# Kernel optimization log

Measured on AMD Instinct MI355X. Metric: run time of the kernel, lower is better.

## Reference

```python
import jax, jax.numpy as jnp
import numpy as np

B, T, C, H, D, W = 4, 4096, 1024, 16, 64, 128  # batch, seq, n_embd, n_head, head_dim, window
NB = T // W  # number of query blocks
EPS = 1e-6


def _rms(x, w):
    # RMSNorm over last dim
    return x * jax.lax.rsqrt(jnp.mean(x * x, axis=-1, keepdims=True) + EPS) * w


def _rope(x, pos_ids):
    # MRoPE: pos_ids [T,3]; axis_id maps each freq to one of 3 axes
    inv_freq = 1.0 / (1e6 ** (jnp.arange(0, D, 2, dtype=jnp.float32) / D))  # [D/2]
    axis_id = jnp.arange(D // 2) % 3
    positions = pos_ids[:, axis_id].astype(jnp.float32)  # [T, D/2]
    freqs = positions * inv_freq  # [T, D/2]
    emb = jnp.concatenate([freqs, freqs], axis=-1)  # [T, D]
    cos = jnp.cos(emb)[None, None]  # [1,1,T,D]
    sin = jnp.sin(emb)[None, None]
    x1, x2 = x[..., : D // 2], x[..., D // 2 :]
    rot = jnp.concatenate([-x2, x1], axis=-1)
    return x * cos + rot * sin


def setup_inputs() -> dict:
    key = jax.random.key(0)
    ks = jax.random.split(key, 3)
    x = jax.random.normal(ks[0], (B, T, C), jnp.float32)
    pos = jnp.arange(T, dtype=jnp.int32)
    pos_ids = jnp.stack([pos, pos, pos], axis=-1)  # [T,3] text positions
    w_attn = jax.random.normal(ks[1], (C, C + 2 * D), jnp.float32) * 0.02
    w_proj = jax.random.normal(ks[2], (C, C), jnp.float32) * 0.02
    q_norm_w = jnp.ones((D,), jnp.float32)
    k_norm_w = jnp.ones((D,), jnp.float32)
    return {"x": x, "pos_ids": pos_ids, "w_attn": w_attn, "w_proj": w_proj,
            "q_norm_w": q_norm_w, "k_norm_w": k_norm_w}


def reference(x, pos_ids, w_attn, w_proj, q_norm_w, k_norm_w):
    # fused qkv projection (torch Linear without bias; weight stored [in,out])
    qkv = x @ w_attn  # [B,T,C+2D]
    q = qkv[..., :C].reshape(B, T, H, D).transpose(0, 2, 1, 3)  # [B,H,T,D]
    k = qkv[..., C : C + D][:, None]  # [B,1,T,D] single KV head (MQA)
    v = qkv[..., C + D :][:, None]  # [B,1,T,D]
    q = _rope(_rms(q, q_norm_w), pos_ids)
    k = _rope(_rms(k, k_norm_w), pos_ids)
    # sliding-window attention (q >= kv and q - kv <= W), computed in blocks of W
    qb = q.reshape(B, H, NB, W, D)
    kb = k.reshape(B, NB, W, D)
    vb = v.reshape(B, NB, W, D)
    kp = jnp.concatenate([jnp.zeros_like(kb[:, :1]), kb[:, :-1]], axis=1)  # prev k block
    vp = jnp.concatenate([jnp.zeros_like(vb[:, :1]), vb[:, :-1]], axis=1)
    kv_k = jnp.concatenate([kp, kb], axis=2)  # [B,NB,2W,D]
    kv_v = jnp.concatenate([vp, vb], axis=2)
    n = jnp.arange(NB)[:, None, None]
    qr = jnp.arange(W)[None, :, None]
    kr = jnp.arange(2 * W)[None, None, :]
    q_abs = n * W + qr
    kv_abs = (n - 1) * W + kr
    mask = (q_abs >= kv_abs) & (q_abs - kv_abs <= W) & (kv_abs >= 0)  # [NB,W,2W]
    scores = jnp.einsum("bhnqd,bnkd->bhnqk", qb, kv_k) / jnp.sqrt(jnp.float32(D))
    scores = jnp.where(mask[None, None], scores, -1e30)
    attn = jax.nn.softmax(scores, axis=-1)
    y = jnp.einsum("bhnqk,bnkd->bhnqd", attn, kv_v)  # [B,H,NB,W,D]
    y = y.reshape(B, H, T, D).transpose(0, 2, 1, 3).reshape(B, T, C)
    return y @ w_proj
```

## Files before the change

kernel.cpp:

```cpp
#include <hip/hip_runtime.h>


typedef __attribute__((ext_vector_type(8))) short short8;
typedef __attribute__((ext_vector_type(4))) float f32x4;
typedef __attribute__((ext_vector_type(16))) float f32x16;
typedef __attribute__((ext_vector_type(4))) unsigned uint4v;

#define DEV static __device__ __forceinline__

DEV unsigned short f2bf(float f) {
  unsigned u = __builtin_bit_cast(unsigned, f);
  u += 0x7fffu + ((u >> 16) & 1u);
  return (unsigned short)(u >> 16);
}
DEV float bf2f(unsigned short s) {
  unsigned u = ((unsigned)s) << 16;
  return __builtin_bit_cast(float, u);
}
DEV unsigned cvtpk(float a, float b) {
  unsigned r;
  asm("v_cvt_pk_bf16_f32 %0, %1, %2" : "=v"(r) : "v"(a), "v"(b));
  return r;
}

DEV f32x4 mfma16(short8 a, short8 b, f32x4 c) {
  return __builtin_amdgcn_mfma_f32_16x16x32_bf16(a, b, c, 0, 0, 0);
}
DEV f32x16 mfma32(short8 a, short8 b, f32x16 c) {
  return __builtin_amdgcn_mfma_f32_32x32x16_bf16(a, b, c, 0, 0, 0);
}

DEV void gload16(const void* g, void* l) {
  __builtin_amdgcn_global_load_lds(
      (const __attribute__((address_space(1))) unsigned int*)(unsigned long long)g,
      (__attribute__((address_space(3))) unsigned int*)(unsigned int)(unsigned long long)l,
      16, 0, 0);
}

__global__ __launch_bounds__(256) void k_prep(const float* __restrict__ x,
                                              short* __restrict__ xb,
                                              const float* __restrict__ wa,
                                              short* __restrict__ wabt,
                                              const float* __restrict__ wp,
                                              short* __restrict__ wpbt,
                                              const int* __restrict__ pos,
                                              float* __restrict__ trig) {
  __shared__ float tl[32][33];
  int bid = blockIdx.x, tid = threadIdx.x;
  if (bid < 16384) {
    int i = bid * 256 + tid;
    float4 v = ((const float4*)x)[i];
    short4 o;
    o.x = (short)f2bf(v.x); o.y = (short)f2bf(v.y);
    o.z = (short)f2bf(v.z); o.w = (short)f2bf(v.w);
    ((short4*)xb)[i] = o;
    return;
  }
  if (bid < 16384 + 1152 + 1024) {
    const float* W; short* Wt; int N, local;
    if (bid < 16384 + 1152) { local = bid - 16384; W = wa; Wt = wabt; N = 1152; }
    else { local = bid - 16384 - 1152; W = wp; Wt = wpbt; N = 1024; }
    int k0 = (local & 31) * 32, n0 = (local >> 5) * 32;
    int tx = tid & 31, ty = tid >> 5;
#pragma unroll
    for (int i = 0; i < 4; ++i)
      tl[ty + i * 8][tx] = W[(size_t)(k0 + ty + i * 8) * N + n0 + tx];
    __syncthreads();
#pragma unroll
    for (int i = 0; i < 4; ++i)
      Wt[(size_t)(n0 + ty + i * 8) * 1024 + k0 + tx] = (short)f2bf(tl[tx][ty + i * 8]);
    return;
  }
  {
    int idx = (bid - 16384 - 1152 - 1024) * 256 + tid;
    int t = idx >> 5, j = idx & 31;
    float invf = __expf((float)j * (-13.815510558f / 32.f));
    float p = (float)pos[t * 3 + (j % 3)];
    float s, c;
    sincosf(p * invf, &s, &c);
    ((float2*)trig)[idx] = make_float2(c, s);
  }
}

__global__ __launch_bounds__(256) void k_gemmkv(const short* __restrict__ A,
                                                const short* __restrict__ Bt,
                                                const float* __restrict__ trig,
                                                const float* __restrict__ kw,
                                                short* __restrict__ kb2,
                                                short* __restrict__ vtg) {
  __shared__ short As[128 * 32];
  __shared__ short Bs[128 * 32];
  const int K = 1024;
  int bid = blockIdx.x;
  int bm = (bid & 7) * 16 + (bid >> 3);
  int tid = threadIdx.x, lane = tid & 63, wid = tid >> 6;
  int wr = wid >> 1, wc = wid & 1;
  int lo = lane & 15, hi = lane >> 4;
  const short* Ab = A + (size_t)(bm * 128 + (tid >> 2)) * K + (tid & 3) * 8;
  const short* Bb = Bt + (size_t)(tid >> 2) * K + (tid & 3) * 8;
  f32x4 acc[4][4] = {};
  for (int kt = 0; kt < K; kt += 32) {
    gload16(Ab + kt,            As + tid * 8);
    gload16(Ab + kt + 64 * K,   As + 2048 + tid * 8);
    gload16(Bb + kt,            Bs + tid * 8);
    gload16(Bb + kt + 64 * K,   Bs + 2048 + tid * 8);
    __syncthreads();
    short8 a[4], b[4];
#pragma unroll
    for (int m = 0; m < 4; ++m)
      a[m] = *(const short8*)&As[(wr * 64 + m * 16 + lo) * 32 + hi * 8];
#pragma unroll
    for (int n = 0; n < 4; ++n)
      b[n] = *(const short8*)&Bs[(wc * 64 + n * 16 + lo) * 32 + hi * 8];
#pragma unroll
    for (int m = 0; m < 4; ++m)
#pragma unroll
      for (int n = 0; n < 4; ++n)
        acc[m][n] = mfma16(a[m], b[n], acc[m][n]);
    __syncthreads();
  }
  int tg0 = (bm * 128 + wr * 64) & 4095;
  int bb  = (bm * 128) >> 12;
  if (wc == 0) {
    float w0 = kw[lo], w1 = kw[16 + lo], w2 = kw[32 + lo], w3 = kw[48 + lo];
    const float2* tb = (const float2*)trig;
#pragma unroll
    for (int m = 0; m < 4; ++m)
#pragma unroll
      for (int r = 0; r < 4; ++r) {
        float x0 = acc[m][0][r], x1 = acc[m][1][r];
        float x2 = acc[m][2][r], x3 = acc[m][3][r];
        float ss = x0 * x0 + x1 * x1 + x2 * x2 + x3 * x3;
        ss += __shfl_xor(ss, 1); ss += __shfl_xor(ss, 2);
        ss += __shfl_xor(ss, 4); ss += __shfl_xor(ss, 8);
        float rn = rsqrtf(ss * 0.015625f + 1e-6f);
        x0 *= rn * w0; x1 *= rn * w1; x2 *= rn * w2; x3 *= rn * w3;
        int tp = tg0 + m * 16 + hi * 4 + r;
        float2 cs0 = tb[tp * 32 + lo];
        float2 cs1 = tb[tp * 32 + 16 + lo];
        float o0 = x0 * cs0.x - x2 * cs0.y;
        float o1 = x1 * cs1.x - x3 * cs1.y;
        float o2 = x2 * cs0.x + x0 * cs0.y;
        float o3 = x3 * cs1.x + x1 * cs1.y;
        size_t tb_ = ((size_t)bb * 4096 + tp) * 64;
        kb2[tb_ + lo]      = (short)f2bf(o0);
        kb2[tb_ + 16 + lo] = (short)f2bf(o1);
        kb2[tb_ + 32 + lo] = (short)f2bf(o2);
        kb2[tb_ + 48 + lo] = (short)f2bf(o3);
      }
  } else {
#pragma unroll
    for (int m = 0; m < 4; ++m)
#pragma unroll
      for (int nf = 0; nf < 4; ++nf) {
        int dd = nf * 16 + lo;
        short4 o;
        o.x = (short)f2bf(acc[m][nf][0]);
        o.y = (short)f2bf(acc[m][nf][1]);
        o.z = (short)f2bf(acc[m][nf][2]);
        o.w = (short)f2bf(acc[m][nf][3]);
        *(short4*)&vtg[((size_t)(bb * 64 + dd)) * 4096 + tg0 + m * 16 + hi * 4] = o;
      }
  }
}

__global__ __launch_bounds__(512, 2) void k_gemm256(
    const short* __restrict__ A, const short* __restrict__ Bt,
    void* __restrict__ Cout, int M, int N, int K, int outBf16,
    const float* __restrict__ trig, const float* __restrict__ qw,
    short* __restrict__ qb2, int mode) {
  __shared__ short sm[65536];
  int nbn = N >> 8;
  int nwg = (M >> 8) * nbn;
  int bid = blockIdx.x;
  int swz = (bid & 7) * (nwg >> 3) + (bid >> 3);
  int bm = swz / nbn, bn = swz % nbn;
  int tid = threadIdx.x, wid = tid >> 6, lane = tid & 63;
  int wm = wid >> 2, wn = wid & 3;
  int lo = lane & 15, hi = lane >> 4;
  int NT = K >> 6;

  int r0 = tid >> 3, dc = tid & 7;
  int sc = dc ^ (r0 & 7);
  const short* aS0 = A  + (size_t)(bm * 256 + r0) * K + sc * 8;
  const short* bS0 = Bt + (size_t)(bn * 256 + r0) * K + sc * 8;
  size_t hstep = (size_t)128 * K;

  auto stageAll = [&](int jt, int d) {
#pragma unroll
    for (int mat = 0; mat < 2; ++mat)
#pragma unroll
      for (int h = 0; h < 2; ++h) {
        const short* s = (mat ? bS0 : aS0) + (size_t)h * hstep + jt * 64;
        short* l = sm + d * 32768 + mat * 16384 + h * 8192;
        gload16(s,                  l + tid * 8);
        gload16(s + (size_t)64 * K, l + 4096 + tid * 8);
      }
  };

  int aRd[2];
#pragma unroll
  for (int kk = 0; kk < 2; ++kk)
    aRd[kk] = lo * 64 + (((kk << 2) | hi) ^ (lo & 7)) * 8;

  short8 Afr[8][2];
  short8 Bfr[4][2];
  f32x4 acc[8][4] = {};

  auto rdA = [&](int d, int m0) {
    int base = d * 32768 + wm * 8192;
#pragma unroll
    for (int m = 0; m < 4; ++m)
#pragma unroll
      for (int kk = 0; kk < 2; ++kk)
        Afr[m0 + m][kk] = *(const short8*)&sm[base + (m0 + m) * 1024 + aRd[kk]];
  };
  auto rdB = [&](int d, int n0) {
    int base = d * 32768 + 16384 + (wn >> 1) * 8192 + (wn & 1) * 4096;
#pragma unroll
    for (int nf = 0; nf < 2; ++nf)
#pragma unroll
      for (int kk = 0; kk < 2; ++kk)
        Bfr[n0 + nf][kk] = *(const short8*)&sm[base + (n0 + nf) * 1024 + aRd[kk]];
  };
  auto quad = [&](int m0, int n0) {
    __builtin_amdgcn_s_setprio(1);
#pragma unroll
    for (int m = 0; m < 4; ++m)
#pragma unroll
      for (int j = 0; j < 2; ++j)
#pragma unroll
        for (int kk = 0; kk < 2; ++kk)
          acc[m0 + m][n0 + j] = mfma16(Afr[m0 + m][kk], Bfr[n0 + j][kk],
                                       acc[m0 + m][n0 + j]);
    __builtin_amdgcn_s_setprio(0);
  };

  stageAll(0, 0);
  __syncthreads();

#pragma unroll 2
  for (int jt = 0; jt < NT; ++jt) {
    int d = jt & 1;
    if (jt + 1 < NT) stageAll(jt + 1, d ^ 1);
    rdA(d, 0); rdB(d, 0); rdB(d, 2);
    quad(0, 0); quad(0, 2);
    rdA(d, 4);
    quad(4, 0); quad(4, 2);
    __syncthreads();
  }

  if (mode == 1) {
    int tg0 = (bm * 256 + wm * 128) & 4095;
    int bb  = (bm * 256) >> 12;
    int hh  = bn * 4 + wn;
    float w0 = qw[lo], w1 = qw[16 + lo], w2 = qw[32 + lo], w3 = qw[48 + lo];
    short* dst = qb2 + (size_t)((bb * 16 + hh) * 4096) * 64;
    const float2* tb = (const float2*)trig;
#pragma unroll
    for (int m = 0; m < 8; ++m)
#pragma unroll
      for (int r = 0; r < 4; ++r) {
        float x0 = acc[m][0][r], x1 = acc[m][1][r];
        float x2 = acc[m][2][r], x3 = acc[m][3][r];
        float ss = x0 * x0 + x1 * x1 + x2 * x2 + x3 * x3;
        ss += __shfl_xor(ss, 1); ss += __shfl_xor(ss, 2);
        ss += __shfl_xor(ss, 4); ss += __shfl_xor(ss, 8);
        float rn = rsqrtf(ss * 0.015625f + 1e-6f);
        x0 *= rn * w0; x1 *= rn * w1; x2 *= rn * w2; x3 *= rn * w3;
        int tp = tg0 + m * 16 + hi * 4 + r;
        float2 cs0 = tb[tp * 32 + lo];
        float2 cs1 = tb[tp * 32 + 16 + lo];
        float o0 = x0 * cs0.x - x2 * cs0.y;
        float o1 = x1 * cs1.x - x3 * cs1.y;
        float o2 = x2 * cs0.x + x0 * cs0.y;
        float o3 = x3 * cs1.x + x1 * cs1.y;
        size_t tb_ = (size_t)tp * 64;
        dst[tb_ + lo]      = (short)f2bf(o0);
        dst[tb_ + 16 + lo] = (short)f2bf(o1);
        dst[tb_ + 32 + lo] = (short)f2bf(o2);
        dst[tb_ + 48 + lo] = (short)f2bf(o3);
      }
    return;
  }

  int row0 = bm * 256 + wm * 128 + hi * 4;
  int col0 = bn * 256 + wn * 64 + lo;
  if (outBf16) {
    short* C = (short*)Cout;
#pragma unroll
    for (int m = 0; m < 8; ++m)
#pragma unroll
      for (int nf = 0; nf < 4; ++nf)
#pragma unroll
        for (int r = 0; r < 4; ++r)
          C[(size_t)(row0 + m * 16 + r) * N + col0 + nf * 16] = (short)f2bf(acc[m][nf][r]);
  } else {
    float* C = (float*)Cout;
#pragma unroll
    for (int m = 0; m < 8; ++m)
#pragma unroll
      for (int nf = 0; nf < 4; ++nf)
#pragma unroll
        for (int r = 0; r < 4; ++r)
          C[(size_t)(row0 + m * 16 + r) * N + col0 + nf * 16] = acc[m][nf][r];
  }
}

__global__ __launch_bounds__(256, 4) void k_attn(const short* __restrict__ qb,
                                                 const short* __restrict__ kb,
                                                 const short* __restrict__ vtg,
                                                 short* __restrict__ y) {
  __shared__ __align__(16) char smem[33792];
  short* ks  = (short*)smem;
  short* vts = (short*)(smem + 16384);
  int bid = blockIdx.x;
  int swz = (bid & 7) * 256 + (bid >> 3);
  int h = swz & 15, n = (swz >> 4) & 31, b = swz >> 9;
  int tid = threadIdx.x, wid = tid >> 6, lane = tid & 63;
  int lo = lane & 31, hi = lane >> 5;

  const short* qrow = qb + (size_t)((b * 16 + h) * 4096 + n * 128 + wid * 32 + lo) * 64;
  short8 aq[4];
#pragma unroll
  for (int s = 0; s < 4; ++s) aq[s] = *(const short8*)(qrow + s * 16 + hi * 8);

  f32x16 O0 = {}, O1 = {};
  float mrun = -1e30f, lrun = 0.f;
  int qr = wid * 32 + lo;
  const float SC = 0.125f * 1.4426950408889634f;

  for (int hf = (n == 0) ? 1 : 0; hf < 2; ++hf) {
    int tg = (n - 1 + hf) * 128;
#pragma unroll
    for (int p = 0; p < 4; ++p) {
      int idx = p * 256 + tid;
      int r = idx >> 3, dc = idx & 7;
      gload16(kb + (size_t)(b * 4096 + tg + r) * 64 + ((dc ^ (r & 7)) << 3),
              ks + idx * 8);
    }
#pragma unroll
    for (int p = 0; p < 4; ++p) {
      int idx = p * 256 + tid;
      int dd = idx >> 4, s = idx & 15;
      gload16(vtg + (size_t)(b * 64 + dd) * 4096 + tg + ((s ^ (dd & 7)) << 3),
              vts + idx * 8);
    }
    __syncthreads();

#pragma unroll
    for (int mt = 0; mt < 4; ++mt) {
      f32x16 S = {};
      int r = mt * 32 + lo;
#pragma unroll
      for (int kst = 0; kst < 4; ++kst) {
        short8 kf = *(const short8*)&ks[r * 64 + ((((kst << 1) | hi) ^ (r & 7)) << 3)];
        S = mfma32(kf, aq[kst], S);
      }
#pragma unroll
      for (int rr = 0; rr < 16; ++rr) {
        int kg = hf * 128 + mt * 32 + (rr & 3) + ((rr >> 2) << 3) + (hi << 2);
        S[rr] = (kg >= qr && kg <= qr + 128) ? S[rr] * SC : -30000.f;
      }
      float pmax = S[0];
#pragma unroll
      for (int rr = 1; rr < 16; ++rr) pmax = fmaxf(pmax, S[rr]);
      pmax = fmaxf(pmax, __shfl_xor(pmax, 32));
      if (!__all(pmax - mrun <= 8.f)) {
        float mn = fmaxf(mrun, pmax);
        float al = exp2f(mrun - mn);
        lrun *= al; mrun = mn;
#pragma unroll
        for (int rr = 0; rr < 16; ++rr) { O0[rr] *= al; O1[rr] *= al; }
      }
      float ls = 0.f;
#pragma unroll
      for (int rr = 0; rr < 16; ++rr) { S[rr] = exp2f(S[rr] - mrun); ls += S[rr]; }
      ls += __shfl_xor(ls, 32);
      lrun += ls;
#pragma unroll
      for (int h2 = 0; h2 < 2; ++h2) {
        int b0 = h2 * 8;
        unsigned pk0 = cvtpk(S[b0 + 0], S[b0 + 1]);
        unsigned pk1 = cvtpk(S[b0 + 2], S[b0 + 3]);
        unsigned pk2 = cvtpk(S[b0 + 4], S[b0 + 5]);
        unsigned pk3 = cvtpk(S[b0 + 6], S[b0 + 7]);
        asm("v_permlane32_swap_b32 %0, %1" : "+v"(pk0), "+v"(pk2));
        asm("v_permlane32_swap_b32 %0, %1" : "+v"(pk1), "+v"(pk3));
        uint4v uw; uw.x = pk0; uw.y = pk1; uw.z = pk2; uw.w = pk3;
        short8 pb = __builtin_bit_cast(short8, uw);
        int kc = mt * 4 + h2 * 2 + hi;
        short8 vb0 = *(const short8*)&vts[lo * 128 + ((kc ^ (lo & 7)) << 3)];
        short8 vb1 = *(const short8*)&vts[(32 + lo) * 128 + ((kc ^ (lo & 7)) << 3)];
        O0 = mfma32(vb0, pb, O0);
        O1 = mfma32(vb1, pb, O1);
      }
    }
    __syncthreads();
  }

  float inv = 1.f / lrun;
  float* ot = (float*)smem + wid * 2112;
#pragma unroll
  for (int r = 0; r < 16; ++r) {
    int d0 = (r & 3) + ((r >> 2) << 3) + (hi << 2);
    ot[d0 * 33 + lo]        = O0[r] * inv;
    ot[(d0 + 32) * 33 + lo] = O1[r] * inv;
  }
  __syncthreads();
  int tok = lane >> 3, dc = lane & 7;
#pragma unroll
  for (int g = 0; g < 4; ++g) {
    int q = g * 8 + tok;
    short8 o8;
#pragma unroll
    for (int jj = 0; jj < 8; ++jj)
      o8[jj] = (short)f2bf(ot[(dc * 8 + jj) * 33 + q]);
    *(short8*)&y[(size_t)(b * 4096 + n * 128 + wid * 32 + q) * 1024 + h * 64 + dc * 8] = o8;
  }
}

extern "C" void kernel_launch(void* const* d_in, const int* in_sizes, int n_in,
                              void* d_out, int out_size, void* d_ws, size_t ws_size,
                              hipStream_t stream) {
  const float* x      = (const float*)d_in[0];
  const int*   pos    = (const int*)d_in[1];
  const float* w_attn = (const float*)d_in[2];
  const float* w_proj = (const float*)d_in[3];
  const float* qw     = (const float*)d_in[4];
  const float* kw     = (const float*)d_in[5];

  char* ws = (char*)d_ws;
  short* xb   = (short*)ws;
  short* wabt = (short*)(ws + 33554432);
  short* wpbt = (short*)(ws + 35913728);
  short* qb2  = (short*)(ws + 38010880);
  short* kb2  = (short*)(ws + 71565312);
  short* vtg  = (short*)(ws + 73662464);
  float* trig = (float*)(ws + 75759616);
  short* ybuf = xb;

  hipLaunchKernelGGL(k_prep, dim3(16384 + 1152 + 1024 + 512), dim3(256), 0, stream,
                     x, xb, w_attn, wabt, w_proj, wpbt, pos, trig);
  hipLaunchKernelGGL(k_gemmkv, dim3(128), dim3(256), 0, stream, xb,
                     wabt + (size_t)1024 * 1024, trig, kw, kb2, vtg);
  hipLaunchKernelGGL(k_gemm256, dim3(256), dim3(512), 0, stream, xb, wabt,
                     (void*)nullptr, 16384, 1024, 1024, 1, trig, qw, qb2, 1);
  hipLaunchKernelGGL(k_attn, dim3(2048), dim3(256), 0, stream, qb2, kb2, vtg, ybuf);
  hipLaunchKernelGGL(k_gemm256, dim3(256), dim3(512), 0, stream, ybuf, wpbt, d_out,
                     16384, 1024, 1024, 0,
                     (const float*)nullptr, (const float*)nullptr,
                     (short*)nullptr, 0);
}
```

Measured before the change: 160.2 us.

## Interleave GEMM tile loads with MFMA quads using explicit barriers and waitcnts

Measured after the change: 164.8 us. 1.03x slower.

```diff
diff --git a/kernel.cpp b/kernel.cpp
--- a/kernel.cpp
+++ b/kernel.cpp
@@ -36,6 +36,18 @@
       (__attribute__((address_space(3))) unsigned int*)(unsigned int)(unsigned long long)l,
       16, 0, 0);
 }
+
+DEV short8 dsr128(unsigned a) {
+  short8 r;
+  asm volatile("ds_read_b128 %0, %1" : "=v"(r) : "v"(a));
+  return r;
+}
+
+#define ASMBAR do { asm volatile("s_barrier" ::: "memory"); } while (0)
+#define LGKM0  asm volatile("s_waitcnt lgkmcnt(0)" ::: "memory")
+#define VMCNT2 asm volatile("s_waitcnt vmcnt(2)" ::: "memory")
+#define VMCNT4 asm volatile("s_waitcnt vmcnt(4)" ::: "memory")
+#define SCHED0 __builtin_amdgcn_sched_barrier(0)
 
 __global__ __launch_bounds__(256) void k_prep(const float* __restrict__ x,
                                               short* __restrict__ xb,
@@ -186,42 +198,38 @@
   const short* bS0 = Bt + (size_t)(bn * 256 + r0) * K + sc * 8;
   size_t hstep = (size_t)128 * K;
 
-  auto stageAll = [&](int jt, int d) {
-#pragma unroll
-    for (int mat = 0; mat < 2; ++mat)
-#pragma unroll
-      for (int h = 0; h < 2; ++h) {
-        const short* s = (mat ? bS0 : aS0) + (size_t)h * hstep + jt * 64;
-        short* l = sm + d * 32768 + mat * 16384 + h * 8192;
-        gload16(s,                  l + tid * 8);
-        gload16(s + (size_t)64 * K, l + 4096 + tid * 8);
-      }
+  auto stage = [&](int jt, int mat, int h, int d) {
+    const short* s = (mat ? bS0 : aS0) + (size_t)h * hstep + jt * 64;
+    short* l = sm + d * 32768 + mat * 16384 + h * 8192;
+    gload16(s,                  l + tid * 8);
+    gload16(s + (size_t)64 * K, l + 4096 + tid * 8);
   };
 
-  int aRd[2];
+  unsigned smB = (unsigned)(unsigned long long)(void*)sm;
+  unsigned aRdB[2];
 #pragma unroll
   for (int kk = 0; kk < 2; ++kk)
-    aRd[kk] = lo * 64 + (((kk << 2) | hi) ^ (lo & 7)) * 8;
+    aRdB[kk] = (unsigned)(lo * 128 + (((kk << 2) | hi) ^ (lo & 7)) * 16);
 
   short8 Afr[8][2];
   short8 Bfr[4][2];
   f32x4 acc[8][4] = {};
 
   auto rdA = [&](int d, int m0) {
-    int base = d * 32768 + wm * 8192;
+    unsigned base = smB + d * 65536 + wm * 16384;
 #pragma unroll
     for (int m = 0; m < 4; ++m)
 #pragma unroll
       for (int kk = 0; kk < 2; ++kk)
-        Afr[m0 + m][kk] = *(const short8*)&sm[base + (m0 + m) * 1024 + aRd[kk]];
+        Afr[m0 + m][kk] = dsr128(base + (m0 + m) * 2048 + aRdB[kk]);
   };
   auto rdB = [&](int d, int n0) {
-    int base = d * 32768 + 16384 + (wn >> 1) * 8192 + (wn & 1) * 4096;
+    unsigned base = smB + d * 65536 + 32768 + (wn >> 1) * 16384 + (wn & 1) * 8192;
 #pragma unroll
     for (int nf = 0; nf < 2; ++nf)
 #pragma unroll
       for (int kk = 0; kk < 2; ++kk)
-        Bfr[n0 + nf][kk] = *(const short8*)&sm[base + (n0 + nf) * 1024 + aRd[kk]];
+        Bfr[n0 + nf][kk] = dsr128(base + (n0 + nf) * 2048 + aRdB[kk]);
   };
   auto quad = [&](int m0, int n0) {
     __builtin_amdgcn_s_setprio(1);
@@ -236,18 +244,34 @@
     __builtin_amdgcn_s_setprio(0);
   };
 
-  stageAll(0, 0);
-  __syncthreads();
+  stage(0, 0, 0, 0); stage(0, 1, 0, 0); stage(0, 0, 1, 0); stage(0, 1, 1, 0);
+  if (NT > 1) { stage(1, 0, 0, 1); stage(1, 1, 0, 1); }
+  VMCNT4;
+  ASMBAR;
 
 #pragma unroll 2
   for (int jt = 0; jt < NT; ++jt) {
     int d = jt & 1;
-    if (jt + 1 < NT) stageAll(jt + 1, d ^ 1);
-    rdA(d, 0); rdB(d, 0); rdB(d, 2);
-    quad(0, 0); quad(0, 2);
+    rdA(d, 0); rdB(d, 0);
+    if (jt + 1 < NT) stage(jt + 1, 0, 1, d ^ 1);
+    ASMBAR; LGKM0; SCHED0;
+    quad(0, 0);
+    ASMBAR;
     rdA(d, 4);
-    quad(4, 0); quad(4, 2);
-    __syncthreads();
+    if (jt + 1 < NT) stage(jt + 1, 1, 1, d ^ 1);
+    ASMBAR; LGKM0; SCHED0;
+    quad(4, 0);
+    ASMBAR;
+    rdB(d, 2);
+    if (jt + 2 < NT) stage(jt + 2, 0, 0, d);
+    ASMBAR; LGKM0; SCHED0;
+    quad(0, 2);
+    ASMBAR;
+    if (jt + 2 < NT) stage(jt + 2, 1, 0, d);
+    VMCNT2;
+    ASMBAR;
+    quad(4, 2);
+    ASMBAR;
   }
 
   if (mode == 1) {
```

## Shrink GEMM tile to 256x128 with 4 warps and single-buffered LDS

Applied to the files above, without the earlier changes.

Result: no change. 160.7 us (median of 2 runs) (+0.4%).

```diff
diff --git a/kernel.cpp b/kernel.cpp
--- a/kernel.cpp
+++ b/kernel.cpp
@@ -164,64 +164,51 @@
   }
 }
 
-__global__ __launch_bounds__(512, 2) void k_gemm256(
+__global__ __launch_bounds__(256, 2) void k_gemmbig(
     const short* __restrict__ A, const short* __restrict__ Bt,
     void* __restrict__ Cout, int M, int N, int K, int outBf16,
     const float* __restrict__ trig, const float* __restrict__ qw,
     short* __restrict__ qb2, int mode) {
-  __shared__ short sm[65536];
-  int nbn = N >> 8;
+  __shared__ short sm[24576];
+  int nbn = N >> 7;
   int nwg = (M >> 8) * nbn;
   int bid = blockIdx.x;
   int swz = (bid & 7) * (nwg >> 3) + (bid >> 3);
   int bm = swz / nbn, bn = swz % nbn;
   int tid = threadIdx.x, wid = tid >> 6, lane = tid & 63;
-  int wm = wid >> 2, wn = wid & 3;
+  int wm = wid >> 1, wn = wid & 1;
   int lo = lane & 15, hi = lane >> 4;
   int NT = K >> 6;
 
-  int r0 = tid >> 3, dc = tid & 7;
-  int sc = dc ^ (r0 & 7);
+  int r0 = tid >> 3, ch = tid & 7;
+  int sc = ch ^ (r0 & 7);
   const short* aS0 = A  + (size_t)(bm * 256 + r0) * K + sc * 8;
-  const short* bS0 = Bt + (size_t)(bn * 256 + r0) * K + sc * 8;
-  size_t hstep = (size_t)128 * K;
-
-  auto stageAll = [&](int jt, int d) {
-#pragma unroll
-    for (int mat = 0; mat < 2; ++mat)
-#pragma unroll
-      for (int h = 0; h < 2; ++h) {
-        const short* s = (mat ? bS0 : aS0) + (size_t)h * hstep + jt * 64;
-        short* l = sm + d * 32768 + mat * 16384 + h * 8192;
-        gload16(s,                  l + tid * 8);
-        gload16(s + (size_t)64 * K, l + 4096 + tid * 8);
-      }
-  };
+  const short* bS0 = Bt + (size_t)(bn * 128 + r0) * K + sc * 8;
 
   int aRd[2];
 #pragma unroll
   for (int kk = 0; kk < 2; ++kk)
-    aRd[kk] = lo * 64 + (((kk << 2) | hi) ^ (lo & 7)) * 8;
+    aRd[kk] = (((kk << 2) | hi) ^ (lo & 7)) * 8;
 
   short8 Afr[8][2];
   short8 Bfr[4][2];
   f32x4 acc[8][4] = {};
 
-  auto rdA = [&](int d, int m0) {
-    int base = d * 32768 + wm * 8192;
+  auto rdA = [&](int m0) {
 #pragma unroll
     for (int m = 0; m < 4; ++m)
 #pragma unroll
       for (int kk = 0; kk < 2; ++kk)
-        Afr[m0 + m][kk] = *(const short8*)&sm[base + (m0 + m) * 1024 + aRd[kk]];
+        Afr[m0 + m][kk] =
+            *(const short8*)&sm[(wm * 128 + (m0 + m) * 16 + lo) * 64 + aRd[kk]];
   };
-  auto rdB = [&](int d, int n0) {
-    int base = d * 32768 + 16384 + (wn >> 1) * 8192 + (wn & 1) * 4096;
-#pragma unroll
-    for (int nf = 0; nf < 2; ++nf)
+  auto rdB = [&]() {
+#pragma unroll
+    for (int nf = 0; nf < 4; ++nf)
 #pragma unroll
       for (int kk = 0; kk < 2; ++kk)
-        Bfr[n0 + nf][kk] = *(const short8*)&sm[base + (n0 + nf) * 1024 + aRd[kk]];
+        Bfr[nf][kk] =
+            *(const short8*)&sm[16384 + (wn * 64 + nf * 16 + lo) * 64 + aRd[kk]];
   };
   auto quad = [&](int m0, int n0) {
     __builtin_amdgcn_s_setprio(1);
@@ -236,24 +223,24 @@
     __builtin_amdgcn_s_setprio(0);
   };
 
-  stageAll(0, 0);
-  __syncthreads();
-
-#pragma unroll 2
   for (int jt = 0; jt < NT; ++jt) {
-    int d = jt & 1;
-    if (jt + 1 < NT) stageAll(jt + 1, d ^ 1);
-    rdA(d, 0); rdB(d, 0); rdB(d, 2);
-    quad(0, 0); quad(0, 2);
-    rdA(d, 4);
-    quad(4, 0); quad(4, 2);
+#pragma unroll
+    for (int k = 0; k < 8; ++k)
+      gload16(aS0 + jt * 64 + (size_t)32 * k * K, sm + (tid + k * 256) * 8);
+#pragma unroll
+    for (int k = 0; k < 4; ++k)
+      gload16(bS0 + jt * 64 + (size_t)32 * k * K,
+              sm + 16384 + (tid + k * 256) * 8);
+    __syncthreads();
+    rdA(0); rdB(); rdA(4);
+    quad(0, 0); quad(0, 2); quad(4, 0); quad(4, 2);
     __syncthreads();
   }
 
   if (mode == 1) {
     int tg0 = (bm * 256 + wm * 128) & 4095;
     int bb  = (bm * 256) >> 12;
-    int hh  = bn * 4 + wn;
+    int hh  = bn * 2 + wn;
     float w0 = qw[lo], w1 = qw[16 + lo], w2 = qw[32 + lo], w3 = qw[48 + lo];
     short* dst = qb2 + (size_t)((bb * 16 + hh) * 4096) * 64;
     const float2* tb = (const float2*)trig;
@@ -285,7 +272,7 @@
   }
 
   int row0 = bm * 256 + wm * 128 + hi * 4;
-  int col0 = bn * 256 + wn * 64 + lo;
+  int col0 = bn * 128 + wn * 64 + lo;
   if (outBf16) {
     short* C = (short*)Cout;
 #pragma unroll
@@ -444,10 +431,10 @@
                      x, xb, w_attn, wabt, w_proj, wpbt, pos, trig);
   hipLaunchKernelGGL(k_gemmkv, dim3(128), dim3(256), 0, stream, xb,
                      wabt + (size_t)1024 * 1024, trig, kw, kb2, vtg);
-  hipLaunchKernelGGL(k_gemm256, dim3(256), dim3(512), 0, stream, xb, wabt,
+  hipLaunchKernelGGL(k_gemmbig, dim3(512), dim3(256), 0, stream, xb, wabt,
                      (void*)nullptr, 16384, 1024, 1024, 1, trig, qw, qb2, 1);
   hipLaunchKernelGGL(k_attn, dim3(2048), dim3(256), 0, stream, qb2, kb2, vtg, ybuf);
-  hipLaunchKernelGGL(k_gemm256, dim3(256), dim3(512), 0, stream, ybuf, wpbt, d_out,
+  hipLaunchKernelGGL(k_gemmbig, dim3(512), dim3(256), 0, stream, ybuf, wpbt, d_out,
                      16384, 1024, 1024, 0,
                      (const float*)nullptr, (const float*)nullptr,
                      (short*)nullptr, 0);
```
